# Performance work log

Hardware: AMD Instinct MI355X
Metric: run time of the kernel (lower is better)

The kernel has to match this reference:

```python
import jax, jax.numpy as jnp
import numpy as np
from jax import lax

STRIDE = 16
SCALES = (8.0, 16.0, 32.0)
RATIOS = (0.5, 1.0, 2.0)
PRE_NMS = 6000
POST_NMS = 300
NMS_THRESH = 0.7
MIN_SIZE = 16.0
DN = ('NCHW', 'OIHW', 'NCHW')


def _base_anchors():
    # 9 base anchors centered at (STRIDE/2, STRIDE/2), (ymin,xmin,ymax,xmax)
    c = STRIDE / 2.0
    rows = []
    for r in RATIOS:
        for s in SCALES:
            h = STRIDE * s * np.sqrt(r)
            w = STRIDE * s * np.sqrt(1.0 / r)
            rows.append([c - h / 2, c - w / 2, c + h / 2, c + w / 2])
    return jnp.asarray(np.array(rows, np.float32))


def _all_anchors(wdim, hdim):
    # shift base anchors over the (w, h) feature grid, matching permute(0,2,3,1) flatten order
    sy = jnp.arange(wdim, dtype=jnp.float32) * STRIDE
    sx = jnp.arange(hdim, dtype=jnp.float32) * STRIDE
    yy, xx = jnp.meshgrid(sy, sx, indexing='ij')
    shifts = jnp.stack([yy, xx, yy, xx], axis=-1).reshape(-1, 4)  # [w*h, 4]
    return (shifts[:, None, :] + _base_anchors()[None, :, :]).reshape(-1, 4)  # [w*h*9, 4]


def _conv(x, W, b, pad):
    y = lax.conv_general_dilated(x, W, (1, 1), pad, dimension_numbers=DN)
    return y + b[None, :, None, None]


def _nms_fixed(boxes, keep):
    # sequential greedy NMS over score-sorted boxes; returns POST_NMS boxes (zero padded)
    y1, x1, y2, x2 = boxes[:, 0], boxes[:, 1], boxes[:, 2], boxes[:, 3]
    areas = (y2 - y1) * (x2 - x1)
    N = boxes.shape[0]
    idxs = jnp.arange(N)

    def body(i, keep):
        yy1 = jnp.maximum(y1[i], y1)
        xx1 = jnp.maximum(x1[i], x1)
        yy2 = jnp.minimum(y2[i], y2)
        xx2 = jnp.minimum(x2[i], x2)
        inter = jnp.maximum(yy2 - yy1, 0.0) * jnp.maximum(xx2 - xx1, 0.0)
        iou = inter / (areas[i] + areas - inter + 1e-12)
        suppress = (iou > NMS_THRESH) & (idxs > i) & keep[i]
        return keep & ~suppress

    keep = lax.fori_loop(0, N, body, keep)
    rank = jnp.cumsum(keep) - 1
    slot = jnp.where(keep & (rank < POST_NMS), rank, POST_NMS)  # overflow slot
    out = jnp.zeros((POST_NMS + 1, 4), boxes.dtype).at[slot].set(boxes)
    return out[:POST_NMS]


def _proposals(loc, score_fg, anchors, img_h, img_w):
    ah = anchors[:, 2] - anchors[:, 0]
    aw = anchors[:, 3] - anchors[:, 1]
    acy = anchors[:, 0] + 0.5 * ah
    acx = anchors[:, 1] + 0.5 * aw
    cy = loc[:, 0] * ah + acy
    cx = loc[:, 1] * aw + acx
    h = jnp.exp(loc[:, 2]) * ah
    w = jnp.exp(loc[:, 3]) * aw
    boxes = jnp.stack([cy - 0.5 * h, cx - 0.5 * w, cy + 0.5 * h, cx + 0.5 * w], axis=-1)
    hi = jnp.array([img_h, img_w, img_h, img_w], dtype=boxes.dtype)
    boxes = jnp.clip(boxes, 0.0, hi)
    hs = boxes[:, 2] - boxes[:, 0]
    ws = boxes[:, 3] - boxes[:, 1]
    valid = (hs >= MIN_SIZE) & (ws >= MIN_SIZE)
    sc = jnp.where(valid, score_fg, -jnp.inf)
    top_sc, top_idx = lax.top_k(sc, PRE_NMS)
    cand = boxes[top_idx]
    return _nms_fixed(cand, jnp.isfinite(top_sc))


def setup_inputs() -> dict:
    key = jax.random.key(0)
    k = jax.random.split(key, 4)
    return {
        'base_feature_map': jax.random.normal(k[0], (8, 512, 50, 50), jnp.float32),
        'W_conv': jax.random.normal(k[1], (512, 512, 3, 3), jnp.float32) * 0.01,
        'b_conv': jnp.zeros((512,), jnp.float32),
        'W_cls': jax.random.normal(k[2], (18, 512, 1, 1), jnp.float32) * 0.01,
        'b_cls': jnp.zeros((18,), jnp.float32),
        'W_reg': jax.random.normal(k[3], (36, 512, 1, 1), jnp.float32) * 0.01,
        'b_reg': jnp.zeros((36,), jnp.float32),
        'img_h': 800,
        'img_w': 800,
    }


def reference(base_feature_map, W_conv, b_conv, W_cls, b_cls, W_reg, b_reg, img_h, img_w):
    n, _, w, h = base_feature_map.shape
    anchors = _all_anchors(w, h)  # [w*h*9, 4]
    x = jax.nn.relu(_conv(base_feature_map, W_conv, b_conv, 'SAME'))
    rpn_locs = _conv(x, W_reg, b_reg, 'VALID').transpose(0, 2, 3, 1).reshape(n, -1, 4)
    rpn_scores = _conv(x, W_cls, b_cls, 'VALID').transpose(0, 2, 3, 1).reshape(n, -1, 2)
    fg = jax.nn.softmax(rpn_scores[0], axis=-1)[:, 1]
    rois = _proposals(rpn_locs[0], fg, anchors, float(img_h), float(img_w))
    return rpn_locs, rpn_scores, anchors, rois
```

## Files before the change

### kernel.cpp

```cpp
#include <hip/hip_runtime.h>
#include <cstdint>
#include <math.h>

typedef unsigned int u32;
typedef unsigned long long u64;
typedef __attribute__((ext_vector_type(8))) short short8v;
typedef __attribute__((ext_vector_type(4))) float f32x4;

#define N_BATCH 8
#define C_IN    512
#define PX      2500
#define KDIM    4608
#define NA      22500
#define PRE_NMS 6000
#define POST_NMS 300

#define OUT_SCORES 720000
#define OUT_ANCH   1080000
#define OUT_ROIS   1170000

#define WS_X     0
#define WS_SCORE 10240000
#define WS_BOX   10262500
#define WS_LIST  10352500
#define WS_META  10388500
#define WS_WP    10388608
#define WS_XP    12747904
#define WS_END   22987904

#define NW_ELEMS (512 * KDIM)
#define NX_ELEMS (N_BATCH * C_IN * PX)

__device__ inline u32 rne_hi16(float f) {
    u32 u = __float_as_uint(f);
    return (u + 0x7FFFu + ((u >> 16) & 1u)) >> 16;
}
__device__ inline u32 pack_split(float f) {
    u32 rh  = rne_hi16(f);
    float d = f - __uint_as_float(rh << 16);
    u32 rl  = rne_hi16(d);
    return (rh << 16) | rl;
}

__global__ __launch_bounds__(256) void k_prep(const float* __restrict__ Wc,
                                              const float* __restrict__ in,
                                              u32* __restrict__ WP,
                                              u32* __restrict__ XP) {
    int o = blockIdx.x * 256 + threadIdx.x;
    if (o < NW_ELEMS) {
        int ci_in = o & 31;
        int tmp   = o >> 5;
        int r     = tmp % 9;
        int cc    = tmp / 9;
        int co    = cc >> 4;
        int cig   = cc & 15;
        int ci    = cig * 32 + ci_in;
        WP[o] = pack_split(Wc[(size_t)co * KDIM + ci * 9 + r]);
    } else {
        int o2 = o - NW_ELEMS;
        if (o2 < NX_ELEMS && XP) XP[o2] = pack_split(in[o2]);
    }
}

__global__ __launch_bounds__(256) void k_conv3(const float* __restrict__ in,
                                               const u32* __restrict__ XP,
                                               const u32* __restrict__ WP,
                                               const float* __restrict__ bc,
                                               float* __restrict__ xout) {
    __shared__ unsigned short AsH[128][40];
    __shared__ unsigned short AsL[128][40];
    __shared__ unsigned short BsH[128][40];
    __shared__ unsigned short BsL[128][40];

    int b  = blockIdx.x;
    int n  = b & 7;
    int q  = b >> 3;
    int cb = q & 3;
    int pt = q >> 2;
    int t  = threadIdx.x;
    int lane = t & 63;
    int w  = t >> 6;
    int wr = w >> 1, wc = w & 1;
    int px0 = pt * 128, co0 = cb * 128;
    const float* inN = in + (size_t)n * C_IN * PX;
    const u32*   XPn = XP ? (XP + (size_t)n * C_IN * PX) : nullptr;

    int sco = t >> 1;
    int skb = (t & 1) << 4;
    int spx = t & 127;
    int skk = (t >> 7) << 4;
    int gpx = px0 + spx;
    int sy  = gpx / 50;
    int sx  = gpx - sy * 50;
    bool pxok = (gpx < PX);
    const u32* wpA = WP + (size_t)(co0 + sco) * KDIM + skb;

    f32x4 acc[4][4];
#pragma unroll
    for (int i = 0; i < 4; ++i)
#pragma unroll
        for (int j = 0; j < 4; ++j) acc[i][j] = (f32x4)0.f;

    const int ro = lane & 15;
    const int g8 = (lane >> 4) << 3;

    for (int cig = 0; cig < 16; ++cig) {
        int ci0 = cig << 5;
        for (int r = 0; r < 9; ++r) {
            int kstep = cig * 9 + r;
            {
                const u32* wp = wpA + kstep * 32;
                u32 uu[16];
                *(uint4*)&uu[0]  = *(const uint4*)(wp);
                *(uint4*)&uu[4]  = *(const uint4*)(wp + 4);
                *(uint4*)&uu[8]  = *(const uint4*)(wp + 8);
                *(uint4*)&uu[12] = *(const uint4*)(wp + 12);
                short8v v0, v1, u0, u1;
#pragma unroll
                for (int e = 0; e < 8; ++e) {
                    v0[e] = (short)(uu[e] >> 16);
                    v1[e] = (short)(uu[8 + e] >> 16);
                    u0[e] = (short)(uu[e] & 0xFFFFu);
                    u1[e] = (short)(uu[8 + e] & 0xFFFFu);
                }
                *(short8v*)&AsH[sco][skb]     = v0;
                *(short8v*)&AsH[sco][skb + 8] = v1;
                *(short8v*)&AsL[sco][skb]     = u0;
                *(short8v*)&AsL[sco][skb + 8] = u1;
            }
            {
                int ry = (r * 11) >> 5;
                int dy = ry - 1;
                int dx = r - ry * 3 - 1;
                int iy = sy + dy, ix = sx + dx;
                bool valid = pxok && ((unsigned)iy < 50u) && ((unsigned)ix < 50u);
                int off = iy * 50 + ix;
                short8v v0, v1, u0, u1;
                if (XPn) {
                    const u32* bp = XPn + (size_t)(ci0 + skk) * PX + off;
                    u32 uu[16];
#pragma unroll
                    for (int it = 0; it < 16; ++it)
                        uu[it] = valid ? bp[it * PX] : 0u;
#pragma unroll
                    for (int e = 0; e < 8; ++e) {
                        v0[e] = (short)(uu[e] >> 16);
                        v1[e] = (short)(uu[8 + e] >> 16);
                        u0[e] = (short)(uu[e] & 0xFFFFu);
                        u1[e] = (short)(uu[8 + e] & 0xFFFFu);
                    }
                } else {
                    const float* bp = inN + (size_t)(ci0 + skk) * PX + off;
                    float bv[16];
#pragma unroll
                    for (int it = 0; it < 16; ++it)
                        bv[it] = valid ? bp[it * PX] : 0.f;
#pragma unroll
                    for (int e = 0; e < 8; ++e) {
                        u32 pa = pack_split(bv[e]);
                        u32 pb = pack_split(bv[8 + e]);
                        v0[e] = (short)(pa >> 16);
                        v1[e] = (short)(pb >> 16);
                        u0[e] = (short)(pa & 0xFFFFu);
                        u1[e] = (short)(pb & 0xFFFFu);
                    }
                }
                *(short8v*)&BsH[spx][skk]     = v0;
                *(short8v*)&BsH[spx][skk + 8] = v1;
                *(short8v*)&BsL[spx][skk]     = u0;
                *(short8v*)&BsL[spx][skk + 8] = u1;
            }
            __syncthreads();

            short8v aH[4], aL[4], bH[4], bL[4];
#pragma unroll
            for (int s = 0; s < 4; ++s) {
                aH[s] = *(const short8v*)&AsH[wr * 64 + s * 16 + ro][g8];
                aL[s] = *(const short8v*)&AsL[wr * 64 + s * 16 + ro][g8];
                bH[s] = *(const short8v*)&BsH[wc * 64 + s * 16 + ro][g8];
                bL[s] = *(const short8v*)&BsL[wc * 64 + s * 16 + ro][g8];
            }
#pragma unroll
            for (int i = 0; i < 4; ++i)
#pragma unroll
                for (int j = 0; j < 4; ++j) {
                    acc[i][j] = __builtin_amdgcn_mfma_f32_16x16x32_bf16(aH[i], bH[j], acc[i][j], 0, 0, 0);
                    acc[i][j] = __builtin_amdgcn_mfma_f32_16x16x32_bf16(aH[i], bL[j], acc[i][j], 0, 0, 0);
                    acc[i][j] = __builtin_amdgcn_mfma_f32_16x16x32_bf16(aL[i], bH[j], acc[i][j], 0, 0, 0);
                }
            __syncthreads();
        }
    }

    int coB  = co0 + wr * 64;
    int pxB  = px0 + wc * 64 + ro;
    int rowg = (lane >> 4) << 2;
#pragma unroll
    for (int i = 0; i < 4; ++i) {
#pragma unroll
        for (int rg = 0; rg < 4; ++rg) {
            int co = coB + i * 16 + rowg + rg;
            float bias = bc[co];
            float* dst = xout + ((size_t)n * C_IN + co) * PX;
#pragma unroll
            for (int j = 0; j < 4; ++j) {
                int px = pxB + j * 16;
                if (px < PX) dst[px] = fmaxf(acc[i][j][rg] + bias, 0.f);
            }
        }
    }
}

__device__ inline float readDim(const void* p) {
    int v = *(const int*)p;
    if (v > 0 && v <= 100000) return (float)v;
    return *(const float*)p;
}

__global__ __launch_bounds__(256) void k_heads(const float* __restrict__ x,
                                               const float* __restrict__ Wreg,
                                               const float* __restrict__ breg,
                                               const float* __restrict__ Wcls,
                                               const float* __restrict__ bcls,
                                               float* __restrict__ out,
                                               float* __restrict__ wsScore,
                                               float* __restrict__ wsBox,
                                               const void* pih, const void* piw) {
    __shared__ float As[32][68];
    __shared__ float Bs[32][132];
    __shared__ float Hs[54][132];
    int b  = blockIdx.x;
    int pt = b % 20, n = b / 20;
    int t  = threadIdx.x;
    int tx = t & 15, ty = t >> 4;
    int px0 = pt * 128;
    float acc[4][8];
#pragma unroll
    for (int i = 0; i < 4; ++i)
#pragma unroll
        for (int j = 0; j < 8; ++j) acc[i][j] = 0.f;

    for (int k0 = 0; k0 < 512; k0 += 32) {
        {
            int c   = t >> 2;
            int kkb = (t & 3) << 3;
            const float* src = nullptr;
            if (c < 36)      src = Wreg + (size_t)c * 512 + k0 + kkb;
            else if (c < 54) src = Wcls + (size_t)(c - 36) * 512 + k0 + kkb;
#pragma unroll
            for (int qq = 0; qq < 2; ++qq) {
                float4 wv = src ? *(const float4*)(src + qq * 4) : make_float4(0, 0, 0, 0);
                As[kkb + qq * 4 + 0][c] = wv.x;
                As[kkb + qq * 4 + 1][c] = wv.y;
                As[kkb + qq * 4 + 2][c] = wv.z;
                As[kkb + qq * 4 + 3][c] = wv.w;
            }
        }
        {
            int pxl = t & 127;
            int kk0 = (t >> 7) << 4;
            int px  = px0 + pxl;
#pragma unroll
            for (int it = 0; it < 16; ++it) {
                int kk = kk0 + it;
                float v = 0.f;
                if (px < PX) v = x[((size_t)n * 512 + k0 + kk) * PX + px];
                Bs[kk][pxl] = v;
            }
        }
        __syncthreads();
#pragma unroll 8
        for (int kk = 0; kk < 32; ++kk) {
            float a[4], bb[8];
            *(float4*)&a[0]  = *(const float4*)&As[kk][ty * 4];
            *(float4*)&bb[0] = *(const float4*)&Bs[kk][tx * 8];
            *(float4*)&bb[4] = *(const float4*)&Bs[kk][tx * 8 + 4];
#pragma unroll
            for (int i = 0; i < 4; ++i)
#pragma unroll
                for (int j = 0; j < 8; ++j)
                    acc[i][j] = fmaf(a[i], bb[j], acc[i][j]);
        }
        __syncthreads();
    }
    int pxb = px0 + tx * 8;
#pragma unroll
    for (int i = 0; i < 4; ++i) {
        int c = ty * 4 + i;
        if (c >= 54) continue;
        float bias = (c < 36) ? breg[c] : bcls[c - 36];
        for (int j = 0; j < 8; ++j) {
            int px = pxb + j;
            if (px >= PX) break;
            float v = acc[i][j] + bias;
            if (c < 36)
                out[(size_t)n * 90000 + (size_t)px * 36 + c] = v;
            else
                out[OUT_SCORES + (size_t)n * 45000 + (size_t)px * 18 + (c - 36)] = v;
            if (n == 0) Hs[c][tx * 8 + j] = v;
        }
    }

    if (n == 0) {
        __syncthreads();
        float imgH = readDim(pih), imgW = readDim(piw);
        const float ratios[3] = {0.5f, 1.f, 2.f};
        const float scales[3] = {8.f, 16.f, 32.f};
        for (int idx = t; idx < 128 * 9; idx += 256) {
            int pxl = idx / 9;
            int a   = idx - pxl * 9;
            int px  = px0 + pxl;
            if (px >= PX) continue;
            int gi = px * 9 + a;
            int y = px / 50, xq = px - y * 50;
            float r = ratios[a / 3], s = scales[a % 3];
            float hh = 16.f * s * sqrtf(r);
            float wv = 16.f * s * sqrtf(1.f / r);
            float ay1 = y * 16.f + 8.f - 0.5f * hh;
            float ax1 = xq * 16.f + 8.f - 0.5f * wv;
            float ay2 = y * 16.f + 8.f + 0.5f * hh;
            float ax2 = xq * 16.f + 8.f + 0.5f * wv;
            *(float4*)(out + OUT_ANCH + (size_t)gi * 4) = make_float4(ay1, ax1, ay2, ax2);

            float l0 = Hs[a * 4 + 0][pxl];
            float l1 = Hs[a * 4 + 1][pxl];
            float l2 = Hs[a * 4 + 2][pxl];
            float l3 = Hs[a * 4 + 3][pxl];
            float s0 = Hs[36 + 2 * a][pxl];
            float s1 = Hs[37 + 2 * a][pxl];
            float fg = 1.f / (1.f + expf(s0 - s1));
            float ah = ay2 - ay1, aw = ax2 - ax1;
            float acy = ay1 + 0.5f * ah, acx = ax1 + 0.5f * aw;
            float cy = l0 * ah + acy;
            float cx = l1 * aw + acx;
            float bh = expf(l2) * ah;
            float bw = expf(l3) * aw;
            float b0 = cy - 0.5f * bh, b1 = cx - 0.5f * bw;
            float b2 = cy + 0.5f * bh, b3 = cx + 0.5f * bw;
            b0 = fminf(fmaxf(b0, 0.f), imgH);
            b1 = fminf(fmaxf(b1, 0.f), imgW);
            b2 = fminf(fmaxf(b2, 0.f), imgH);
            b3 = fminf(fmaxf(b3, 0.f), imgW);
            bool valid = ((b2 - b0) >= 16.f) && ((b3 - b1) >= 16.f);
            wsScore[gi] = valid ? fg : -INFINITY;
            *(float4*)(wsBox + (size_t)gi * 4) = make_float4(b0, b1, b2, b3);
        }
    }
}

__device__ inline u32 fkey(float s) {
    u32 u = __float_as_uint(s);
    return (u & 0x80000000u) ? ~u : (u | 0x80000000u);
}

__global__ __launch_bounds__(1024) void k_select(const float* __restrict__ score,
                                                 u64* __restrict__ list,
                                                 int* __restrict__ meta) {
    __shared__ u32 hist[4096];
    __shared__ int sB1, sB2, sM3, sNeed, sV;
    __shared__ u32 sT32;
    __shared__ int cHi, cTie;
    int t = threadIdx.x;
    const int NT = 1024;

    for (int i = t; i < 4096; i += NT) hist[i] = 0;
    __syncthreads();
    for (int i = t; i < NA; i += NT) atomicAdd(&hist[fkey(score[i]) >> 20], 1u);
    __syncthreads();
    for (int off = 1; off < 4096; off <<= 1) {
        u32 v[4]; int c = 0;
        for (int bb = t; bb < 4096; bb += NT) { v[c++] = hist[bb] + ((bb + off < 4096) ? hist[bb + off] : 0u); }
        __syncthreads();
        c = 0;
        for (int bb = t; bb < 4096; bb += NT) hist[bb] = v[c++];
        __syncthreads();
    }
    for (int bb = t; bb < 4096; bb += NT) {
        u32 Sb  = hist[bb];
        u32 Sb1 = (bb < 4095) ? hist[bb + 1] : 0u;
        if (Sb >= PRE_NMS && Sb1 < PRE_NMS) sB1 = bb;
    }
    if (t == 0) sV = (int)hist[2048];
    __syncthreads();
    int B1 = sB1;
    int m1 = (B1 < 4095) ? (int)hist[B1 + 1] : 0;
    int V  = sV;
    __syncthreads();

    for (int i = t; i < 4096; i += NT) hist[i] = 0;
    __syncthreads();
    for (int i = t; i < NA; i += NT) {
        u32 key = fkey(score[i]);
        if ((int)(key >> 20) == B1) atomicAdd(&hist[(key >> 8) & 0xFFFu], 1u);
    }
    __syncthreads();
    for (int off = 1; off < 4096; off <<= 1) {
        u32 v[4]; int c = 0;
        for (int bb = t; bb < 4096; bb += NT) { v[c++] = hist[bb] + ((bb + off < 4096) ? hist[bb + off] : 0u); }
        __syncthreads();
        c = 0;
        for (int bb = t; bb < 4096; bb += NT) hist[bb] = v[c++];
        __syncthreads();
    }
    for (int bb = t; bb < 4096; bb += NT) {
        int Sb  = m1 + (int)hist[bb];
        int Sb1 = m1 + (int)((bb < 4095) ? hist[bb + 1] : 0u);
        if (Sb >= PRE_NMS && Sb1 < PRE_NMS) sB2 = bb;
    }
    __syncthreads();
    int B2 = sB2;
    int m2 = m1 + (int)((B2 < 4095) ? hist[B2 + 1] : 0u);
    u32 P24 = ((u32)B1 << 12) | (u32)B2;
    __syncthreads();

    for (int i = t; i < 256; i += NT) hist[i] = 0;
    __syncthreads();
    for (int i = t; i < NA; i += NT) {
        u32 key = fkey(score[i]);
        if ((key >> 8) == P24) atomicAdd(&hist[key & 0xFFu], 1u);
    }
    __syncthreads();
    for (int off = 1; off < 256; off <<= 1) {
        u32 v[1]; int c = 0;
        for (int bb = t; bb < 256; bb += NT) { v[c++] = hist[bb] + ((bb + off < 256) ? hist[bb + off] : 0u); }
        __syncthreads();
        c = 0;
        for (int bb = t; bb < 256; bb += NT) hist[bb] = v[c++];
        __syncthreads();
    }
    for (int bb = t; bb < 256; bb += NT) {
        int Sb  = m2 + (int)hist[bb];
        int Sb1 = m2 + (int)((bb < 255) ? hist[bb + 1] : 0u);
        if (Sb >= PRE_NMS && Sb1 < PRE_NMS) {
            sM3   = m2 + (int)((bb < 255) ? hist[bb + 1] : 0u);
            sNeed = PRE_NMS - sM3;
            sT32  = (P24 << 8) | (u32)bb;
        }
    }
    if (t == 0) { cHi = 0; cTie = 0; meta[0] = (V < PRE_NMS) ? V : PRE_NMS; }
    __syncthreads();
    int m3 = sM3, need = sNeed;
    u32 T32 = sT32;

    for (int i = t; i < NA; i += NT) {
        u32 key = fkey(score[i]);
        u64 comp = ((u64)key << 32) | (u64)(0xFFFFFFFFu - (u32)i);
        if (key > T32) {
            int p = atomicAdd(&cHi, 1);
            list[p] = comp;
        } else if (key == T32) {
            int p = atomicAdd(&cTie, 1);
            if (p < need) list[m3 + p] = comp;
        }
    }
    for (int i = PRE_NMS + t; i < 8192; i += NT) list[i] = 0ull;
}

__global__ __launch_bounds__(1024) void k_presort(u64* __restrict__ list) {
    __shared__ u64 ls[1024];
    int t  = threadIdx.x;
    int gi = (blockIdx.x << 10) + t;
    ls[t] = list[gi];
    __syncthreads();
    for (int k = 2; k <= 1024; k <<= 1) {
        for (int j = k >> 1; j > 0; j >>= 1) {
            int ixj = t ^ j;
            if (ixj > t) {
                u64 a = ls[t], b = ls[ixj];
                bool desc = ((gi & k) == 0);
                if (desc ? (a < b) : (a > b)) { ls[t] = b; ls[ixj] = a; }
            }
            __syncthreads();
        }
    }
    list[gi] = ls[t];
}

__global__ __launch_bounds__(1024) void k_mergenms(const u64* __restrict__ list,
                                                   const float* __restrict__ boxes,
                                                   const int* __restrict__ meta,
                                                   float* __restrict__ rois) {
    __shared__ u64 sb[8192];
    __shared__ float kb[POST_NMS][4];
    __shared__ float cb4[64][4];
    __shared__ u32 KLo[64], KHi[64], supA[64];
    __shared__ int sKept;
    int t = threadIdx.x;
    const int NT = 1024;

    for (int i = t; i < 8192; i += NT) sb[i] = list[i];
    __syncthreads();

    for (int k = 2048; k <= 8192; k <<= 1) {
        for (int j = k >> 1; j > 0; j >>= 1) {
            for (int i = t; i < 8192; i += NT) {
                int ixj = i ^ j;
                if (ixj > i) {
                    u64 a = sb[i], bv = sb[ixj];
                    bool desc = ((i & k) == 0);
                    if (desc ? (a < bv) : (a > bv)) { sb[i] = bv; sb[ixj] = a; }
                }
            }
            __syncthreads();
        }
    }

    int keepN = meta[0];
    if (t == 0) sKept = 0;
    __syncthreads();

    int s = t >> 4, g = t & 15;
    for (int c0 = 0; c0 < PRE_NMS; c0 += 64) {
        if (sKept >= POST_NMS) break;
        if (t < 64) {
            u32 bidx = 0xFFFFFFFFu - (u32)sb[c0 + t];
            if (bidx >= NA) bidx = 0;
            float4 bx = *(const float4*)(boxes + (size_t)bidx * 4);
            cb4[t][0] = bx.x; cb4[t][1] = bx.y; cb4[t][2] = bx.z; cb4[t][3] = bx.w;
            KLo[t] = 0; KHi[t] = 0; supA[t] = 0;
        }
        __syncthreads();

        float y1 = cb4[s][0], x1 = cb4[s][1], y2 = cb4[s][2], x2 = cb4[s][3];
        float area = (y2 - y1) * (x2 - x1);

        u32 klo = 0, khi = 0;
#pragma unroll
        for (int qq = 0; qq < 4; ++qq) {
            int j = g * 4 + qq;
            if (j > s) {
                float jy1 = cb4[j][0], jx1 = cb4[j][1], jy2 = cb4[j][2], jx2 = cb4[j][3];
                float yy1 = fmaxf(y1, jy1), xx1 = fmaxf(x1, jx1);
                float yy2 = fminf(y2, jy2), xx2 = fminf(x2, jx2);
                float inter = fmaxf(yy2 - yy1, 0.f) * fmaxf(xx2 - xx1, 0.f);
                float ja = (jy2 - jy1) * (jx2 - jx1);
                float iou = inter / (area + ja - inter + 1e-12f);
                if (iou > 0.7f) { if (j < 32) klo |= 1u << j; else khi |= 1u << (j - 32); }
            }
        }
        if (klo) atomicOr(&KLo[s], klo);
        if (khi) atomicOr(&KHi[s], khi);

        int kept0 = sKept;
        bool supf = false;
        for (int jj = g; jj < kept0; jj += 16) {
            float ky1 = kb[jj][0], kx1 = kb[jj][1], ky2 = kb[jj][2], kx2 = kb[jj][3];
            float yy1 = fmaxf(ky1, y1), xx1 = fmaxf(kx1, x1);
            float yy2 = fminf(ky2, y2), xx2 = fminf(kx2, x2);
            float inter = fmaxf(yy2 - yy1, 0.f) * fmaxf(xx2 - xx1, 0.f);
            float karea = (ky2 - ky1) * (kx2 - kx1);
            float iou = inter / (karea + area - inter + 1e-12f);
            if (iou > 0.7f) { supf = true; break; }
        }
        if (supf) atomicOr(&supA[s], 1u);
        __syncthreads();

        if (t == 0) {
            u64 supm = 0;
            int kept = sKept;
            for (int s2 = 0; s2 < 64 && kept < POST_NMS; ++s2) {
                if (c0 + s2 >= keepN) continue;
                if (supA[s2]) continue;
                if ((supm >> s2) & 1ull) continue;
                kb[kept][0] = cb4[s2][0]; kb[kept][1] = cb4[s2][1];
                kb[kept][2] = cb4[s2][2]; kb[kept][3] = cb4[s2][3];
                *(float4*)(rois + (size_t)kept * 4) =
                    make_float4(cb4[s2][0], cb4[s2][1], cb4[s2][2], cb4[s2][3]);
                kept++;
                supm |= ((u64)KHi[s2] << 32) | (u64)KLo[s2];
            }
            sKept = kept;
        }
        __syncthreads();
    }

    int kf = sKept;
    for (int r = kf * 4 + t; r < POST_NMS * 4; r += NT) rois[r] = 0.f;
}

extern "C" void kernel_launch(void* const* d_in, const int* in_sizes, int n_in,
                              void* d_out, int out_size, void* d_ws, size_t ws_size,
                              hipStream_t stream) {
    const float* feat = (const float*)d_in[0];
    const float* Wc   = (const float*)d_in[1];
    const float* bc   = (const float*)d_in[2];
    const float* Wcls = (const float*)d_in[3];
    const float* bcls = (const float*)d_in[4];
    const float* Wreg = (const float*)d_in[5];
    const float* breg = (const float*)d_in[6];
    const void* pih   = d_in[7];
    const void* piw   = d_in[8];
    float* out = (float*)d_out;
    float* ws  = (float*)d_ws;

    u32* WP   = (u32*)(ws + WS_WP);
    u64* list = (u64*)(ws + WS_LIST);
    int* meta = (int*)(ws + WS_META);
    bool haveXP = (ws_size >= (size_t)WS_END * sizeof(float));
    u32* XP = haveXP ? (u32*)(ws + WS_XP) : nullptr;

    int prepItems = NW_ELEMS + (haveXP ? NX_ELEMS : 0);
    hipLaunchKernelGGL(k_prep, dim3((prepItems + 255) / 256), dim3(256), 0, stream, Wc, feat, WP, XP);
    hipLaunchKernelGGL(k_conv3, dim3(640), dim3(256), 0, stream, feat, XP, WP, bc, ws + WS_X);
    hipLaunchKernelGGL(k_heads, dim3(160), dim3(256), 0, stream, ws + WS_X, Wreg, breg, Wcls, bcls,
                       out, ws + WS_SCORE, ws + WS_BOX, pih, piw);
    hipLaunchKernelGGL(k_select, dim3(1), dim3(1024), 0, stream, ws + WS_SCORE, list, meta);
    hipLaunchKernelGGL(k_presort, dim3(8), dim3(1024), 0, stream, list);
    hipLaunchKernelGGL(k_mergenms, dim3(1), dim3(1024), 0, stream, list, ws + WS_BOX, meta, out + OUT_ROIS);
}
```

Baseline: 635.1 us.

## Store packed hi/lo words in swizzled LDS and split them with perm after reading

The conv3x3 split-bf16 GEMM now keeps packed 32-bit hi/lo words in one XOR-swizzled shared tile per operand. Previously it split them into four padded hi/lo short arrays while staging. The split moves to the fragment-read side using v_perm byte selects, and the swizzle is meant to avoid LDS bank conflicts without padding. This cuts staging ALU work and LDS footprint, but adds perm instructions on every fragment load, and each block row is reread by several waves.

```diff
diff --git a/kernel.cpp b/kernel.cpp
--- a/kernel.cpp
+++ b/kernel.cpp
@@ -67,10 +67,8 @@
                                                const u32* __restrict__ WP,
                                                const float* __restrict__ bc,
                                                float* __restrict__ xout) {
-    __shared__ unsigned short AsH[128][40];
-    __shared__ unsigned short AsL[128][40];
-    __shared__ unsigned short BsH[128][40];
-    __shared__ unsigned short BsL[128][40];
+    __shared__ u32 Ap[128][32];
+    __shared__ u32 Bp[128][32];
 
     int b  = blockIdx.x;
     int n  = b & 7;
@@ -101,8 +99,8 @@
 #pragma unroll
         for (int j = 0; j < 4; ++j) acc[i][j] = (f32x4)0.f;
 
-    const int ro = lane & 15;
-    const int g8 = (lane >> 4) << 3;
+    const int ro  = lane & 15;
+    const int g8s = (lane >> 4) << 1;
 
     for (int cig = 0; cig < 16; ++cig) {
         int ci0 = cig << 5;
@@ -110,23 +108,13 @@
             int kstep = cig * 9 + r;
             {
                 const u32* wp = wpA + kstep * 32;
-                u32 uu[16];
-                *(uint4*)&uu[0]  = *(const uint4*)(wp);
-                *(uint4*)&uu[4]  = *(const uint4*)(wp + 4);
-                *(uint4*)&uu[8]  = *(const uint4*)(wp + 8);
-                *(uint4*)&uu[12] = *(const uint4*)(wp + 12);
-                short8v v0, v1, u0, u1;
-#pragma unroll
-                for (int e = 0; e < 8; ++e) {
-                    v0[e] = (short)(uu[e] >> 16);
-                    v1[e] = (short)(uu[8 + e] >> 16);
-                    u0[e] = (short)(uu[e] & 0xFFFFu);
-                    u1[e] = (short)(uu[8 + e] & 0xFFFFu);
+                int rs = sco & 7;
+#pragma unroll
+                for (int qq = 0; qq < 4; ++qq) {
+                    uint4 wv = *(const uint4*)(wp + qq * 4);
+                    int slot = ((skb >> 2) + qq) ^ rs;
+                    *(uint4*)&Ap[sco][slot << 2] = wv;
                 }
-                *(short8v*)&AsH[sco][skb]     = v0;
-                *(short8v*)&AsH[sco][skb + 8] = v1;
-                *(short8v*)&AsL[sco][skb]     = u0;
-                *(short8v*)&AsL[sco][skb + 8] = u1;
             }
             {
                 int ry = (r * 11) >> 5;
@@ -135,50 +123,60 @@
                 int iy = sy + dy, ix = sx + dx;
                 bool valid = pxok && ((unsigned)iy < 50u) && ((unsigned)ix < 50u);
                 int off = iy * 50 + ix;
-                short8v v0, v1, u0, u1;
+                u32 uu[16];
                 if (XPn) {
                     const u32* bp = XPn + (size_t)(ci0 + skk) * PX + off;
-                    u32 uu[16];
 #pragma unroll
                     for (int it = 0; it < 16; ++it)
                         uu[it] = valid ? bp[it * PX] : 0u;
-#pragma unroll
-                    for (int e = 0; e < 8; ++e) {
-                        v0[e] = (short)(uu[e] >> 16);
-                        v1[e] = (short)(uu[8 + e] >> 16);
-                        u0[e] = (short)(uu[e] & 0xFFFFu);
-                        u1[e] = (short)(uu[8 + e] & 0xFFFFu);
-                    }
                 } else {
                     const float* bp = inN + (size_t)(ci0 + skk) * PX + off;
-                    float bv[16];
 #pragma unroll
                     for (int it = 0; it < 16; ++it)
-                        bv[it] = valid ? bp[it * PX] : 0.f;
-#pragma unroll
-                    for (int e = 0; e < 8; ++e) {
-                        u32 pa = pack_split(bv[e]);
-                        u32 pb = pack_split(bv[8 + e]);
-                        v0[e] = (short)(pa >> 16);
-                        v1[e] = (short)(pb >> 16);
-                        u0[e] = (short)(pa & 0xFFFFu);
-                        u1[e] = (short)(pb & 0xFFFFu);
+                        uu[it] = valid ? pack_split(bp[it * PX]) : 0u;
+                }
+                int rs = spx & 7;
+#pragma unroll
+                for (int qq = 0; qq < 4; ++qq) {
+                    int slot = ((skk >> 2) + qq) ^ rs;
+                    *(uint4*)&Bp[spx][slot << 2] = *(uint4*)&uu[qq * 4];
+                }
+            }
+            __syncthreads();
+
+            short8v aH[4], aL[4], bH[4], bL[4];
+#pragma unroll
+            for (int s = 0; s < 4; ++s) {
+                {
+                    int ra = wr * 64 + s * 16 + ro;
+                    int rs = ra & 7;
+                    u32 pa[8];
+                    *(uint4*)&pa[0] = *(const uint4*)&Ap[ra][(g8s ^ rs) << 2];
+                    *(uint4*)&pa[4] = *(const uint4*)&Ap[ra][((g8s + 1) ^ rs) << 2];
+                    u32 h[4], l[4];
+#pragma unroll
+                    for (int w2 = 0; w2 < 4; ++w2) {
+                        h[w2] = __builtin_amdgcn_perm(pa[2 * w2 + 1], pa[2 * w2], 0x07060302u);
+                        l[w2] = __builtin_amdgcn_perm(pa[2 * w2 + 1], pa[2 * w2], 0x05040100u);
                     }
+                    aH[s] = *(short8v*)h;
+                    aL[s] = *(short8v*)l;
                 }
-                *(short8v*)&BsH[spx][skk]     = v0;
-                *(short8v*)&BsH[spx][skk + 8] = v1;
-                *(short8v*)&BsL[spx][skk]     = u0;
-                *(short8v*)&BsL[spx][skk + 8] = u1;
-            }
-            __syncthreads();
-
-            short8v aH[4], aL[4], bH[4], bL[4];
-#pragma unroll
-            for (int s = 0; s < 4; ++s) {
-                aH[s] = *(const short8v*)&AsH[wr * 64 + s * 16 + ro][g8];
-                aL[s] = *(const short8v*)&AsL[wr * 64 + s * 16 + ro][g8];
-                bH[s] = *(const short8v*)&BsH[wc * 64 + s * 16 + ro][g8];
-                bL[s] = *(const short8v*)&BsL[wc * 64 + s * 16 + ro][g8];
+                {
+                    int rb = wc * 64 + s * 16 + ro;
+                    int rs = rb & 7;
+                    u32 pb[8];
+                    *(uint4*)&pb[0] = *(const uint4*)&Bp[rb][(g8s ^ rs) << 2];
+                    *(uint4*)&pb[4] = *(const uint4*)&Bp[rb][((g8s + 1) ^ rs) << 2];
+                    u32 h[4], l[4];
+#pragma unroll
+                    for (int w2 = 0; w2 < 4; ++w2) {
+                        h[w2] = __builtin_amdgcn_perm(pb[2 * w2 + 1], pb[2 * w2], 0x07060302u);
+                        l[w2] = __builtin_amdgcn_perm(pb[2 * w2 + 1], pb[2 * w2], 0x05040100u);
+                    }
+                    bH[s] = *(short8v*)h;
+                    bL[s] = *(short8v*)l;
+                }
             }
 #pragma unroll
             for (int i = 0; i < 4; ++i)
```

After: 639.5 us. No clear change (+0.7%).
